# Kernel optimization log

Measured on AMD Instinct MI355X. Metric: run time of the kernel, lower is better.

Reference implementation:

```python
import jax, jax.numpy as jnp
import numpy as np
import math

N_STATIONS = 50  # N in [N, 7, 56] causal matrix


def setup_inputs() -> dict:
    key = jax.random.key(0)
    k1, k2, k3, k4 = jax.random.split(key, 4)
    B, L, H, E = 3200, 7, 8, 64
    S, D = 56, 64
    queries = jax.random.normal(k1, (B, L, H, E), dtype=jnp.float32)
    keys = jax.random.normal(k2, (B, S, H, E), dtype=jnp.float32)
    values = jax.random.normal(k3, (B, S, H, D), dtype=jnp.float32)
    # station-specific multiplicative causal matrix in [0, 1]
    attn_mask = jax.random.uniform(k4, (N_STATIONS, L, S), dtype=jnp.float32)
    return {"queries": queries, "keys": keys, "values": values, "attn_mask": attn_mask}


def reference(queries, keys, values, attn_mask):
    B, L, H, E = queries.shape
    S = values.shape[1]
    N = attn_mask.shape[0]  # number of stations; B % N == 0
    ab = B // N  # actual batch size per station group
    scale = 1.0 / math.sqrt(E)
    # raw scores [B, H, L, S]
    scores = jnp.einsum('blhe,bshe->bhls', queries, keys)
    # multiplicative station-specific mask: reshape batch into (ab, N) and
    # broadcast mask [N, L, S] over (ab, H)
    masked = scores.reshape(ab, N, H, L, S) * attn_mask[None, :, None, :, :]
    masked = masked.reshape(B, H, L, S)
    # note: scale is applied AFTER masking, as in the original module
    A = jax.nn.softmax(scale * masked, axis=-1)  # dropout is identity at eval
    V = jnp.einsum('bhls,bshd->blhd', A, values)
    return V
```

## Files before the change

### kernel.cpp

```cpp
#include <hip/hip_runtime.h>
#include <math.h>


typedef __attribute__((ext_vector_type(8))) _Float16 half8;

#define GLDS(gp, lp) __builtin_amdgcn_global_load_lds(                        \
    (const __attribute__((address_space(1))) void*)(gp),                      \
    (__attribute__((address_space(3))) void*)(lp), 16, 0, 0)

__launch_bounds__(64, 2)
__global__ void fullattn_kernel(const float* __restrict__ q,
                                const float* __restrict__ k,
                                const float* __restrict__ v,
                                const float* __restrict__ mask,
                                float* __restrict__ out,
                                int nstations) {
    __shared__ __align__(16) float    KL[56 * 64];
    __shared__ __align__(16) _Float16 QL[7 * 64];

    const int lane = threadIdx.x;
    const int unit = blockIdx.x;
    const int b    = unit >> 3;
    const int h    = unit & 7;
    const int st   = b % nstations;

    const int kbase = b * 28672 + h * 64;
    const int qbase = b * 3584  + h * 64;

    const int rr = lane >> 4;
    const int pp = lane & 15;

#pragma unroll
    for (int j = 0; j < 14; ++j) {
        const int row = j * 4 + rr;
        const int c   = pp ^ (row & 15);
        GLDS(k + kbase + row * 512 + c * 4, (char*)KL + j * 1024);
    }
    __builtin_amdgcn_sched_barrier(0);

    float qr[7];
#pragma unroll
    for (int l = 0; l < 7; ++l) qr[l] = q[qbase + l * 512 + lane];
    __builtin_amdgcn_sched_barrier(0);

    const int ml = (lane < 56) ? lane : 55;
    float m[7];
#pragma unroll
    for (int l = 0; l < 7; ++l)
        m[l] = mask[st * 392 + l * 56 + ml] * 0.125f;
    __builtin_amdgcn_sched_barrier(0);

    float vA[8], vB[8], vC[8];
#pragma unroll
    for (int i = 0; i < 8; ++i) vA[i] = v[kbase + i * 512 + lane];
    __builtin_amdgcn_sched_barrier(0);

    asm volatile("s_waitcnt vmcnt(22)" ::: "memory");
    __builtin_amdgcn_sched_barrier(0);

#pragma unroll
    for (int l = 0; l < 7; ++l) QL[l * 64 + lane] = (_Float16)qr[l];

    const int x16 = ml & 15;
    float acc[7];
#pragma unroll
    for (int l = 0; l < 7; ++l) acc[l] = 0.0f;

#pragma unroll
    for (int c2 = 0; c2 < 8; ++c2) {
        const float4 kv0 = *(const float4*)(&KL[ml * 64 + (((2 * c2)     ^ x16) << 2)]);
        const float4 kv1 = *(const float4*)(&KL[ml * 64 + (((2 * c2 + 1) ^ x16) << 2)]);
#pragma unroll
        for (int l = 0; l < 7; ++l) {
            const half8 qv = *(const half8*)(&QL[l * 64 + c2 * 8]);
            acc[l] = fmaf(kv0.x, (float)qv[0], acc[l]);
            acc[l] = fmaf(kv0.y, (float)qv[1], acc[l]);
            acc[l] = fmaf(kv0.z, (float)qv[2], acc[l]);
            acc[l] = fmaf(kv0.w, (float)qv[3], acc[l]);
            acc[l] = fmaf(kv1.x, (float)qv[4], acc[l]);
            acc[l] = fmaf(kv1.y, (float)qv[5], acc[l]);
            acc[l] = fmaf(kv1.z, (float)qv[6], acc[l]);
            acc[l] = fmaf(kv1.w, (float)qv[7], acc[l]);
        }
    }

#pragma unroll
    for (int i = 0; i < 8; ++i) vB[i] = v[kbase + (8 + i) * 512 + lane];
#pragma unroll
    for (int i = 0; i < 8; ++i) vC[i] = v[kbase + (16 + i) * 512 + lane];

    float* pbuf = KL;
    float rdenom[7];
#pragma unroll
    for (int l = 0; l < 7; ++l) {
        const float sc = acc[l] * m[l];
        const float p  = (lane < 56) ? __expf(sc) : 0.0f;
        float sum = p;
#pragma unroll
        for (int off = 32; off >= 1; off >>= 1)
            sum += __shfl_xor(sum, off);
        pbuf[l * 64 + lane] = p;
        rdenom[l] = __builtin_amdgcn_rcpf(sum);
    }

    float facc[7];
#pragma unroll
    for (int l = 0; l < 7; ++l) facc[l] = 0.0f;

    auto pvg = [&](const float (&vw)[8], int g) {
#pragma unroll
        for (int l = 0; l < 7; ++l) {
            const float4 p0 = *(const float4*)(&pbuf[l * 64 + g * 8]);
            const float4 p1 = *(const float4*)(&pbuf[l * 64 + g * 8 + 4]);
            facc[l] = fmaf(p0.x, vw[0], facc[l]);
            facc[l] = fmaf(p0.y, vw[1], facc[l]);
            facc[l] = fmaf(p0.z, vw[2], facc[l]);
            facc[l] = fmaf(p0.w, vw[3], facc[l]);
            facc[l] = fmaf(p1.x, vw[4], facc[l]);
            facc[l] = fmaf(p1.y, vw[5], facc[l]);
            facc[l] = fmaf(p1.z, vw[6], facc[l]);
            facc[l] = fmaf(p1.w, vw[7], facc[l]);
        }
    };
    auto ldv = [&](float (&vw)[8], int row0) {
#pragma unroll
        for (int i = 0; i < 8; ++i) vw[i] = v[kbase + (row0 + i) * 512 + lane];
    };

    pvg(vA, 0); ldv(vA, 24);
    pvg(vB, 1); ldv(vB, 32);
    pvg(vC, 2); ldv(vC, 40);
    pvg(vA, 3); ldv(vA, 48);
    pvg(vB, 4);
    pvg(vC, 5);
    pvg(vA, 6);

#pragma unroll
    for (int l = 0; l < 7; ++l)
        out[qbase + l * 512 + lane] = facc[l] * rdenom[l];
}

extern "C" void kernel_launch(void* const* d_in, const int* in_sizes, int n_in,
                              void* d_out, int out_size, void* d_ws, size_t ws_size,
                              hipStream_t stream) {
    const float* q    = (const float*)d_in[0];
    const float* k    = (const float*)d_in[1];
    const float* v    = (const float*)d_in[2];
    const float* mask = (const float*)d_in[3];
    float* out        = (float*)d_out;

    const int B = in_sizes[0] / (7 * 8 * 64);
    const int nstations = in_sizes[3] / (7 * 56);

    fullattn_kernel<<<dim3(B * 8), dim3(64), 0, stream>>>(q, k, v, mask, out, nstations);
}
```

Before: 166.2 us.

## Stream V through triple-buffered LDS via async global_load_lds and raise occupancy

V rows are now loaded with global_load_lds into a three-slot shared buffer instead of per-lane register loads. The PV loop becomes a software pipeline with explicit vmcnt waits, prefetching the next 8-row chunk while the current one is consumed. Launch bounds go from 2 to 4 waves per SIMD, which the lower register pressure from fewer V registers makes possible. This adds 6KB of LDS per block and depends on hand-counted waitcnt values staying correct.

```diff
diff --git a/kernel.cpp b/kernel.cpp
--- a/kernel.cpp
+++ b/kernel.cpp
@@ -8,7 +8,40 @@
     (const __attribute__((address_space(1))) void*)(gp),                      \
     (__attribute__((address_space(3))) void*)(lp), 16, 0, 0)
 
-__launch_bounds__(64, 2)
+#define PV_STAGE(BUF, CHUNK, WAITN, RC, RB)                                   \
+    asm volatile("s_waitcnt vmcnt(" #WAITN ")" ::: "memory");                 \
+    __builtin_amdgcn_sched_barrier(0);                                        \
+    {                                                                         \
+        float vv[8];                                                          \
+        _Pragma("unroll")                                                     \
+        for (int r = 0; r < 8; ++r) vv[r] = VB[BUF][r * 64 + lane];           \
+        asm volatile("s_waitcnt lgkmcnt(0)" ::: "memory");                    \
+        __builtin_amdgcn_sched_barrier(0);                                    \
+        if ((RC) >= 0) {                                                      \
+            _Pragma("unroll")                                                 \
+            for (int j = 0; j < 2; ++j) {                                     \
+                const int row = (RC) * 8 + j * 4 + rr;                        \
+                GLDS(v + kbase + row * 512 + pp * 4,                          \
+                     (char*)VB[RB] + j * 1024);                               \
+            }                                                                 \
+        }                                                                     \
+        __builtin_amdgcn_sched_barrier(0);                                    \
+        _Pragma("unroll")                                                     \
+        for (int l = 0; l < 7; ++l) {                                         \
+            const float4 p0 = *(const float4*)(&pbuf[l * 64 + (CHUNK) * 8]);  \
+            const float4 p1 = *(const float4*)(&pbuf[l * 64 + (CHUNK) * 8 + 4]); \
+            facc[l] = fmaf(p0.x, vv[0], facc[l]);                             \
+            facc[l] = fmaf(p0.y, vv[1], facc[l]);                             \
+            facc[l] = fmaf(p0.z, vv[2], facc[l]);                             \
+            facc[l] = fmaf(p0.w, vv[3], facc[l]);                             \
+            facc[l] = fmaf(p1.x, vv[4], facc[l]);                             \
+            facc[l] = fmaf(p1.y, vv[5], facc[l]);                             \
+            facc[l] = fmaf(p1.z, vv[6], facc[l]);                             \
+            facc[l] = fmaf(p1.w, vv[7], facc[l]);                             \
+        }                                                                     \
+    }
+
+__launch_bounds__(64, 4)
 __global__ void fullattn_kernel(const float* __restrict__ q,
                                 const float* __restrict__ k,
                                 const float* __restrict__ v,
@@ -16,6 +49,7 @@
                                 float* __restrict__ out,
                                 int nstations) {
     __shared__ __align__(16) float    KL[56 * 64];
+    __shared__ __align__(16) float    VB[3][8 * 64];
     __shared__ __align__(16) _Float16 QL[7 * 64];
 
     const int lane = threadIdx.x;
@@ -50,12 +84,16 @@
         m[l] = mask[st * 392 + l * 56 + ml] * 0.125f;
     __builtin_amdgcn_sched_barrier(0);
 
-    float vA[8], vB[8], vC[8];
 #pragma unroll
-    for (int i = 0; i < 8; ++i) vA[i] = v[kbase + i * 512 + lane];
+    for (int c = 0; c < 3; ++c)
+#pragma unroll
+        for (int j = 0; j < 2; ++j) {
+            const int row = c * 8 + j * 4 + rr;
+            GLDS(v + kbase + row * 512 + pp * 4, (char*)VB[c] + j * 1024);
+        }
     __builtin_amdgcn_sched_barrier(0);
 
-    asm volatile("s_waitcnt vmcnt(22)" ::: "memory");
+    asm volatile("s_waitcnt vmcnt(13)" ::: "memory");
     __builtin_amdgcn_sched_barrier(0);
 
 #pragma unroll
@@ -84,11 +122,6 @@
         }
     }
 
-#pragma unroll
-    for (int i = 0; i < 8; ++i) vB[i] = v[kbase + (8 + i) * 512 + lane];
-#pragma unroll
-    for (int i = 0; i < 8; ++i) vC[i] = v[kbase + (16 + i) * 512 + lane];
-
     float* pbuf = KL;
     float rdenom[7];
 #pragma unroll
@@ -107,33 +140,13 @@
 #pragma unroll
     for (int l = 0; l < 7; ++l) facc[l] = 0.0f;
 
-    auto pvg = [&](const float (&vw)[8], int g) {
-#pragma unroll
-        for (int l = 0; l < 7; ++l) {
-            const float4 p0 = *(const float4*)(&pbuf[l * 64 + g * 8]);
-            const float4 p1 = *(const float4*)(&pbuf[l * 64 + g * 8 + 4]);
-            facc[l] = fmaf(p0.x, vw[0], facc[l]);
-            facc[l] = fmaf(p0.y, vw[1], facc[l]);
-            facc[l] = fmaf(p0.z, vw[2], facc[l]);
-            facc[l] = fmaf(p0.w, vw[3], facc[l]);
-            facc[l] = fmaf(p1.x, vw[4], facc[l]);
-            facc[l] = fmaf(p1.y, vw[5], facc[l]);
-            facc[l] = fmaf(p1.z, vw[6], facc[l]);
-            facc[l] = fmaf(p1.w, vw[7], facc[l]);
-        }
-    };
-    auto ldv = [&](float (&vw)[8], int row0) {
-#pragma unroll
-        for (int i = 0; i < 8; ++i) vw[i] = v[kbase + (row0 + i) * 512 + lane];
-    };
-
-    pvg(vA, 0); ldv(vA, 24);
-    pvg(vB, 1); ldv(vB, 32);
-    pvg(vC, 2); ldv(vC, 40);
-    pvg(vA, 3); ldv(vA, 48);
-    pvg(vB, 4);
-    pvg(vC, 5);
-    pvg(vA, 6);
+    PV_STAGE(0, 0, 4,  3, 0)
+    PV_STAGE(1, 1, 4,  4, 1)
+    PV_STAGE(2, 2, 4,  5, 2)
+    PV_STAGE(0, 3, 4,  6, 0)
+    PV_STAGE(1, 4, 4, -1, 0)
+    PV_STAGE(2, 5, 2, -1, 0)
+    PV_STAGE(0, 6, 0, -1, 0)
 
 #pragma unroll
     for (int l = 0; l < 7; ++l)
```

Result: slower. 195.0 us (+17.3%).
